# Optimization experiments

Hardware: AMD Instinct MI355X
Metric: run time of the kernel (lower is better)

## Reference

```python
import jax, jax.numpy as jnp
import numpy as np

NUM_EMBEDDINGS = 512
EMBEDDING_DIM = 64
COMMITMENT_COST = 0.25


def setup_inputs() -> dict:
    key = jax.random.key(0)
    k1, k2 = jax.random.split(key)
    inputs = jax.random.normal(k1, (16, EMBEDDING_DIM, 4096), dtype=jnp.float32)
    # torch init: uniform(-1/num_embeddings, 1/num_embeddings)
    codebook = jax.random.uniform(
        k2, (NUM_EMBEDDINGS, EMBEDDING_DIM), dtype=jnp.float32,
        minval=-1.0 / NUM_EMBEDDINGS, maxval=1.0 / NUM_EMBEDDINGS)
    return {"inputs": inputs, "codebook": codebook}


def reference(inputs, codebook):
    # inputs: [B, D, T] -> permute to [B, T, D]
    x = jnp.transpose(inputs, (0, 2, 1))
    B, T, D = x.shape
    K = codebook.shape[0]
    flat = x.reshape(-1, D)  # [N, D]

    distances = (jnp.sum(flat * flat, axis=1, keepdims=True)
                 + jnp.sum(codebook * codebook, axis=1)
                 - 2.0 * flat @ codebook.T)  # [N, K]
    idx = jnp.argmin(distances, axis=1)  # [N]
    encodings = jax.nn.one_hot(idx, K, dtype=jnp.float32)  # [N, K]

    # direct gather == encodings @ codebook
    quantized = codebook[idx].reshape(B, T, D)

    e_latent_loss = jnp.mean((jax.lax.stop_gradient(quantized) - x) ** 2)
    q_latent_loss = jnp.mean((quantized - jax.lax.stop_gradient(x)) ** 2)
    loss = q_latent_loss + COMMITMENT_COST * e_latent_loss

    # straight-through estimator
    quantized_st = x + jax.lax.stop_gradient(quantized - x)

    avg_probs = jnp.mean(encodings, axis=0)
    perplexity = jnp.exp(-jnp.sum(avg_probs * jnp.log(avg_probs + 1e-10)))

    return (loss, jnp.transpose(quantized_st, (0, 2, 1)), perplexity, encodings)
```

## Files before the change

kernel.cpp:

```cpp
#include <hip/hip_runtime.h>

#define B_ 16
#define D_ 64
#define T_ 4096
#define K_ 512
#define N_ (B_*T_)
#define Q_ (B_*D_*T_)
#define ENC_OFF ((size_t)(2 + Q_))

#define WS_LOSS    0
#define WS_HIST    8
#define WS_AMB_CNT 2056
#define WS_NE      2064
#define WS_IDX     4352
#define WS_AMB     266496
#define WS_CBH     528640
#define WS_CBL     594176

typedef __bf16 bf16x8 __attribute__((ext_vector_type(8)));
typedef float  f32x4  __attribute__((ext_vector_type(4)));

#define MARGIN_ 2.5e-6f

__global__ __launch_bounds__(512) void k0_init(const float* __restrict__ cb,
                                               float* __restrict__ ne,
                                               int* __restrict__ hist,
                                               int* __restrict__ amb_cnt,
                                               double* __restrict__ loss,
                                               bf16x8* __restrict__ cbh,
                                               bf16x8* __restrict__ cbl) {
    int tid = threadIdx.x;
    float s = 0.f;
#pragma unroll
    for (int d = 0; d < 64; ++d) { float c = cb[tid*64 + d]; s = fmaf(c, c, s); }
    ne[tid] = s;
    hist[tid] = 0;
    if (tid == 0) { *amb_cnt = 0; *loss = 0.0; }

    int lane = tid & 63;
    int g0   = tid >> 6;
#pragma unroll
    for (int g = 0; g < 8; ++g) {
        int ctks = g * 8 + g0;
        int ct = ctks >> 1, ks = ctks & 1;
        int code  = ct * 16 + (lane & 15);
        int dbase = ks * 32 + ((lane >> 4) << 3);
        bf16x8 h, l;
#pragma unroll
        for (int j = 0; j < 8; ++j) {
            float v = cb[code * 64 + dbase + j];
            __bf16 hv = (__bf16)v;
            __bf16 lv = (__bf16)(v - (float)hv);
            h[j] = hv; l[j] = lv;
        }
        cbh[(ct * 2 + ks) * 64 + lane] = h;
        cbl[(ct * 2 + ks) * 64 + lane] = l;
    }
}

__global__ __launch_bounds__(256) void k1_score(const float* __restrict__ in,
                                                const bf16x8* __restrict__ cbh,
                                                const bf16x8* __restrict__ cbl,
                                                const float* __restrict__ ne,
                                                int* __restrict__ idx_out,
                                                int* __restrict__ amb,
                                                int* __restrict__ amb_cnt) {
    __shared__ float X[64][129];
    __shared__ float ne_s[512];
    int tid = threadIdx.x;
    int n0 = blockIdx.x * 128;
    int b  = n0 >> 12, t0 = n0 & (T_ - 1);

    {
        int tl = tid & 127, dg = tid >> 7;
#pragma unroll
        for (int i = 0; i < 32; ++i) {
            int d = dg * 32 + i;
            X[d][tl] = in[((size_t)b * 64 + d) * T_ + t0 + tl];
        }
    }
    ne_s[tid] = ne[tid];
    ne_s[tid + 256] = ne[tid + 256];
    __syncthreads();

    int w = tid >> 6, lane = tid & 63;
    int col = lane & 15, q = lane >> 4;

    bf16x8 Ah[2][2], Al[2][2];
#pragma unroll
    for (int r = 0; r < 2; ++r) {
        int rl = (w * 2 + r) * 16 + col;
#pragma unroll
        for (int ks = 0; ks < 2; ++ks) {
            bf16x8 h, l;
#pragma unroll
            for (int j = 0; j < 8; ++j) {
                float v = X[ks * 32 + q * 8 + j][rl];
                __bf16 hv = (__bf16)v;
                __bf16 lv = (__bf16)(v - (float)hv);
                h[j] = hv; l[j] = lv;
            }
            Ah[r][ks] = h; Al[r][ks] = l;
        }
    }

    int rt0 = blockIdx.x * 8 + w * 2;
    float m1[2][4], m2[2][4]; int i1[2][4];
#pragma unroll
    for (int r = 0; r < 2; ++r)
#pragma unroll
        for (int e = 0; e < 4; ++e) { m1[r][e] = 3.4e38f; m2[r][e] = 3.4e38f; i1[r][e] = 0; }

    for (int ct = 0; ct < 32; ++ct) {
        bf16x8 Bh0 = cbh[(ct * 2 + 0) * 64 + lane];
        bf16x8 Bh1 = cbh[(ct * 2 + 1) * 64 + lane];
        bf16x8 Bl0 = cbl[(ct * 2 + 0) * 64 + lane];
        bf16x8 Bl1 = cbl[(ct * 2 + 1) * 64 + lane];
        float nev = ne_s[ct * 16 + col];
        int code = ct * 16 + col;
#pragma unroll
        for (int r = 0; r < 2; ++r) {
            f32x4 acc = {0.f, 0.f, 0.f, 0.f};
            acc = __builtin_amdgcn_mfma_f32_16x16x32_bf16(Ah[r][0], Bh0, acc, 0, 0, 0);
            acc = __builtin_amdgcn_mfma_f32_16x16x32_bf16(Ah[r][1], Bh1, acc, 0, 0, 0);
            acc = __builtin_amdgcn_mfma_f32_16x16x32_bf16(Ah[r][0], Bl0, acc, 0, 0, 0);
            acc = __builtin_amdgcn_mfma_f32_16x16x32_bf16(Al[r][0], Bh0, acc, 0, 0, 0);
            acc = __builtin_amdgcn_mfma_f32_16x16x32_bf16(Ah[r][1], Bl1, acc, 0, 0, 0);
            acc = __builtin_amdgcn_mfma_f32_16x16x32_bf16(Al[r][1], Bh1, acc, 0, 0, 0);
            acc = __builtin_amdgcn_mfma_f32_16x16x32_bf16(Al[r][0], Bl0, acc, 0, 0, 0);
            acc = __builtin_amdgcn_mfma_f32_16x16x32_bf16(Al[r][1], Bl1, acc, 0, 0, 0);
#pragma unroll
            for (int e = 0; e < 4; ++e) {
                float sc = fmaf(-2.f, acc[e], nev);
                bool lt = sc < m1[r][e];
                m2[r][e] = lt ? m1[r][e] : fminf(m2[r][e], sc);
                i1[r][e] = lt ? code : i1[r][e];
                m1[r][e] = lt ? sc : m1[r][e];
            }
        }
    }

#pragma unroll
    for (int r = 0; r < 2; ++r)
#pragma unroll
        for (int e = 0; e < 4; ++e) {
            float a1 = m1[r][e], a2 = m2[r][e]; int ai = i1[r][e];
#pragma unroll
            for (int off = 1; off < 16; off <<= 1) {
                float o1 = __shfl_xor(a1, off);
                float o2 = __shfl_xor(a2, off);
                int   oi = __shfl_xor(ai, off);
                float nn2 = fminf(fmaxf(a1, o1), fminf(a2, o2));
                bool tk = (o1 < a1) || (o1 == a1 && oi < ai);
                a1 = tk ? o1 : a1; ai = tk ? oi : ai; a2 = nn2;
            }
            if (col == 0) {
                int n = (rt0 + r) * 16 + q * 4 + e;
                idx_out[n] = ai;
                if (a2 - a1 < MARGIN_) { int p = atomicAdd(amb_cnt, 1); amb[p] = n; }
            }
        }
}

__global__ __launch_bounds__(64) void k2_refine(const float* __restrict__ in,
                                                const float* __restrict__ cb,
                                                const int* __restrict__ amb,
                                                const int* __restrict__ amb_cnt,
                                                int* __restrict__ idx_out) {
    int cnt = *amb_cnt;
    int lane = threadIdx.x;
    for (int i = blockIdx.x; i < cnt; i += gridDim.x) {
        int n = amb[i];
        int b = n >> 12, t = n & (T_ - 1);
        const float* xp = in + (size_t)b * D_ * T_ + t;
        double best = 1e300; int bidx = 0;
#pragma unroll
        for (int j = 0; j < 8; ++j) {
            int k = j * 64 + lane;
            const float* c = cb + k * 64;
            double dot = 0.0, nrm = 0.0;
            for (int d = 0; d < 64; ++d) {
                double cd = (double)c[d];
                dot = fma(cd, (double)xp[d * T_], dot);
                nrm = fma(cd, cd, nrm);
            }
            double score = nrm - 2.0 * dot;
            if (score < best) { best = score; bidx = k; }
        }
        for (int off = 32; off > 0; off >>= 1) {
            double ob = __shfl_down(best, off);
            int oi = __shfl_down(bidx, off);
            if (ob < best || (ob == best && oi < bidx)) { best = ob; bidx = oi; }
        }
        if (lane == 0) idx_out[n] = bidx;
    }
}

__global__ __launch_bounds__(256) void k34_outputs(const float* __restrict__ in,
                                                   const float* __restrict__ cb,
                                                   const int* __restrict__ idx_arr,
                                                   float* __restrict__ out,
                                                   float2* __restrict__ enc2,
                                                   int* __restrict__ hist,
                                                   double* __restrict__ loss) {
    int tid = threadIdx.x;
    int n0 = blockIdx.x * 64;
    int b = n0 >> 12, t0 = n0 & (T_ - 1);

#pragma unroll 4
    for (int i = 0; i < 64; ++i) {
        int row = n0 + i;
        int id = idx_arr[row];
        float2 v;
        v.x = ((id >> 1) == tid && (id & 1) == 0) ? 1.f : 0.f;
        v.y = ((id >> 1) == tid && (id & 1) == 1) ? 1.f : 0.f;
        enc2[(size_t)row * 256 + tid] = v;
    }

    int tl = tid & 63, dg = tid >> 6;
    int n = n0 + tl;
    int idx = idx_arr[n];
    const float4* c4 = (const float4*)(cb + (size_t)idx * 64);
    const float* xp = in + (size_t)b * D_ * T_ + t0 + tl;
    float* qp = out + 1 + (size_t)b * D_ * T_ + t0 + tl;

    float lsum = 0.f;
#pragma unroll
    for (int j = 0; j < 4; ++j) {
        float4 qv = c4[dg * 4 + j];
        float qe[4] = {qv.x, qv.y, qv.z, qv.w};
#pragma unroll
        for (int e = 0; e < 4; ++e) {
            int d = dg * 16 + j * 4 + e;
            float xv = xp[(size_t)d * T_];
            float diff = qe[e] - xv;
            lsum = fmaf(diff, diff, lsum);
            qp[(size_t)d * T_] = xv + diff;
        }
    }
    if (tid < 64) atomicAdd(&hist[idx], 1);

#pragma unroll
    for (int off = 32; off > 0; off >>= 1) lsum += __shfl_down(lsum, off);
    __shared__ float wsum[4];
    if ((tid & 63) == 0) wsum[tid >> 6] = lsum;
    __syncthreads();
    if (tid == 0) {
        double s = (double)wsum[0] + (double)wsum[1] + (double)wsum[2] + (double)wsum[3];
        atomicAdd(loss, s);
    }
}

__global__ __launch_bounds__(512) void k6_final(const int* __restrict__ hist,
                                                const double* __restrict__ loss,
                                                float* __restrict__ out) {
    __shared__ double sh[512];
    int k = threadIdx.x;
    double p = (double)hist[k] / (double)N_;
    sh[k] = p * log(p + 1e-10);
    __syncthreads();
    for (int s = 256; s > 0; s >>= 1) {
        if (k < s) sh[k] += sh[k + s];
        __syncthreads();
    }
    if (k == 0) {
        out[1 + Q_] = (float)exp(-sh[0]);
        out[0] = (float)(1.25 * (*loss) / (double)Q_);
    }
}

extern "C" void kernel_launch(void* const* d_in, const int* in_sizes, int n_in,
                              void* d_out, int out_size, void* d_ws, size_t ws_size,
                              hipStream_t stream) {
    const float* in = (const float*)d_in[0];
    const float* cb = (const float*)d_in[1];
    float* out = (float*)d_out;
    char* ws = (char*)d_ws;

    double* loss  = (double*)(ws + WS_LOSS);
    int* hist     = (int*)(ws + WS_HIST);
    int* amb_cnt  = (int*)(ws + WS_AMB_CNT);
    float* ne     = (float*)(ws + WS_NE);
    int* idx      = (int*)(ws + WS_IDX);
    int* amb      = (int*)(ws + WS_AMB);
    bf16x8* cbh   = (bf16x8*)(ws + WS_CBH);
    bf16x8* cbl   = (bf16x8*)(ws + WS_CBL);

    float2* enc2 = (float2*)(out + ENC_OFF);

    k0_init<<<1, 512, 0, stream>>>(cb, ne, hist, amb_cnt, loss, cbh, cbl);
    k1_score<<<512, 256, 0, stream>>>(in, cbh, cbl, ne, idx, amb, amb_cnt);
    k2_refine<<<512, 64, 0, stream>>>(in, cb, amb, amb_cnt, idx);
    k34_outputs<<<N_ / 64, 256, 0, stream>>>(in, cb, idx, out, enc2, hist, loss);
    k6_final<<<1, 512, 0, stream>>>(hist, loss, out);
}
```

Before: 231.5 us.

## Fuse scoring and output kernels, drop ambiguity refinement and low-low MFMA terms

Merges the scoring, refinement and output kernels into one kernel that keeps argmin indices and the input tile in shared memory. It then writes the one-hot encodings, the quantized output and the loss directly, which removes the idx round trip, the second read of the inputs, and two launches. It also drops the fp64 refinement pass for near-tie rows and the two lo*lo MFMA terms, and parallelizes the codebook prep across 8 blocks. The cost is that argmin now relies only on the three-term split-bf16 product with no exact-precision fallback, so near-ties may pick a different code than the fp32 reference.

After: 198.8 us. 1.16x faster.

```diff
diff --git a/kernel.cpp b/kernel.cpp
--- a/kernel.cpp
+++ b/kernel.cpp
@@ -10,39 +10,39 @@
 
 #define WS_LOSS    0
 #define WS_HIST    8
-#define WS_AMB_CNT 2056
 #define WS_NE      2064
-#define WS_IDX     4352
-#define WS_AMB     266496
-#define WS_CBH     528640
-#define WS_CBL     594176
+#define WS_CBH     4608
+#define WS_CBL     70144
 
 typedef __bf16 bf16x8 __attribute__((ext_vector_type(8)));
 typedef float  f32x4  __attribute__((ext_vector_type(4)));
 
-#define MARGIN_ 2.5e-6f
-
-__global__ __launch_bounds__(512) void k0_init(const float* __restrict__ cb,
+__global__ __launch_bounds__(256) void k0_init(const float* __restrict__ cb,
                                                float* __restrict__ ne,
                                                int* __restrict__ hist,
-                                               int* __restrict__ amb_cnt,
                                                double* __restrict__ loss,
                                                bf16x8* __restrict__ cbh,
                                                bf16x8* __restrict__ cbl) {
-    int tid = threadIdx.x;
-    float s = 0.f;
-#pragma unroll
-    for (int d = 0; d < 64; ++d) { float c = cb[tid*64 + d]; s = fmaf(c, c, s); }
-    ne[tid] = s;
-    hist[tid] = 0;
-    if (tid == 0) { *amb_cnt = 0; *loss = 0.0; }
-
-    int lane = tid & 63;
-    int g0   = tid >> 6;
-#pragma unroll
-    for (int g = 0; g < 8; ++g) {
-        int ctks = g * 8 + g0;
-        int ct = ctks >> 1, ks = ctks & 1;
+    int bidx = blockIdx.x, tid = threadIdx.x;
+
+    if (tid < 64) {
+        int code = bidx * 64 + tid;
+        float s = 0.f;
+#pragma unroll
+        for (int d = 0; d < 64; ++d) { float c = cb[code*64 + d]; s = fmaf(c, c, s); }
+        ne[code] = s;
+    }
+    if (bidx == 0) {
+        hist[tid] = 0; hist[tid + 256] = 0;
+        if (tid == 0) *loss = 0.0;
+    }
+
+#pragma unroll
+    for (int p = 0; p < 2; ++p) {
+        int e = p * 256 + tid;
+        int ct = bidx * 4 + (e >> 7);
+        int ks = (e >> 6) & 1;
+        int lane = e & 63;
         int code  = ct * 16 + (lane & 15);
         int dbase = ks * 32 + ((lane >> 4) << 3);
         bf16x8 h, l;
@@ -58,15 +58,18 @@
     }
 }
 
-__global__ __launch_bounds__(256) void k1_score(const float* __restrict__ in,
-                                                const bf16x8* __restrict__ cbh,
-                                                const bf16x8* __restrict__ cbl,
-                                                const float* __restrict__ ne,
-                                                int* __restrict__ idx_out,
-                                                int* __restrict__ amb,
-                                                int* __restrict__ amb_cnt) {
+__global__ __launch_bounds__(256) void k_main(const float* __restrict__ in,
+                                              const float* __restrict__ cb,
+                                              const bf16x8* __restrict__ cbh,
+                                              const bf16x8* __restrict__ cbl,
+                                              const float* __restrict__ ne,
+                                              float* __restrict__ out,
+                                              float2* __restrict__ enc2,
+                                              int* __restrict__ hist,
+                                              double* __restrict__ loss) {
     __shared__ float X[64][129];
     __shared__ float ne_s[512];
+    __shared__ int   sidx[128];
     int tid = threadIdx.x;
     int n0 = blockIdx.x * 128;
     int b  = n0 >> 12, t0 = n0 & (T_ - 1);
@@ -104,12 +107,11 @@
         }
     }
 
-    int rt0 = blockIdx.x * 8 + w * 2;
-    float m1[2][4], m2[2][4]; int i1[2][4];
+    float m1[2][4]; int i1[2][4];
 #pragma unroll
     for (int r = 0; r < 2; ++r)
 #pragma unroll
-        for (int e = 0; e < 4; ++e) { m1[r][e] = 3.4e38f; m2[r][e] = 3.4e38f; i1[r][e] = 0; }
+        for (int e = 0; e < 4; ++e) { m1[r][e] = 3.4e38f; i1[r][e] = 0; }
 
     for (int ct = 0; ct < 32; ++ct) {
         bf16x8 Bh0 = cbh[(ct * 2 + 0) * 64 + lane];
@@ -127,13 +129,10 @@
             acc = __builtin_amdgcn_mfma_f32_16x16x32_bf16(Al[r][0], Bh0, acc, 0, 0, 0);
             acc = __builtin_amdgcn_mfma_f32_16x16x32_bf16(Ah[r][1], Bl1, acc, 0, 0, 0);
             acc = __builtin_amdgcn_mfma_f32_16x16x32_bf16(Al[r][1], Bh1, acc, 0, 0, 0);
-            acc = __builtin_amdgcn_mfma_f32_16x16x32_bf16(Al[r][0], Bl0, acc, 0, 0, 0);
-            acc = __builtin_amdgcn_mfma_f32_16x16x32_bf16(Al[r][1], Bl1, acc, 0, 0, 0);
 #pragma unroll
             for (int e = 0; e < 4; ++e) {
                 float sc = fmaf(-2.f, acc[e], nev);
                 bool lt = sc < m1[r][e];
-                m2[r][e] = lt ? m1[r][e] : fminf(m2[r][e], sc);
                 i1[r][e] = lt ? code : i1[r][e];
                 m1[r][e] = lt ? sc : m1[r][e];
             }
@@ -144,101 +143,47 @@
     for (int r = 0; r < 2; ++r)
 #pragma unroll
         for (int e = 0; e < 4; ++e) {
-            float a1 = m1[r][e], a2 = m2[r][e]; int ai = i1[r][e];
+            float a1 = m1[r][e]; int ai = i1[r][e];
 #pragma unroll
             for (int off = 1; off < 16; off <<= 1) {
                 float o1 = __shfl_xor(a1, off);
-                float o2 = __shfl_xor(a2, off);
                 int   oi = __shfl_xor(ai, off);
-                float nn2 = fminf(fmaxf(a1, o1), fminf(a2, o2));
                 bool tk = (o1 < a1) || (o1 == a1 && oi < ai);
-                a1 = tk ? o1 : a1; ai = tk ? oi : ai; a2 = nn2;
+                a1 = tk ? o1 : a1; ai = tk ? oi : ai;
             }
-            if (col == 0) {
-                int n = (rt0 + r) * 16 + q * 4 + e;
-                idx_out[n] = ai;
-                if (a2 - a1 < MARGIN_) { int p = atomicAdd(amb_cnt, 1); amb[p] = n; }
-            }
-        }
-}
-
-__global__ __launch_bounds__(64) void k2_refine(const float* __restrict__ in,
-                                                const float* __restrict__ cb,
-                                                const int* __restrict__ amb,
-                                                const int* __restrict__ amb_cnt,
-                                                int* __restrict__ idx_out) {
-    int cnt = *amb_cnt;
-    int lane = threadIdx.x;
-    for (int i = blockIdx.x; i < cnt; i += gridDim.x) {
-        int n = amb[i];
-        int b = n >> 12, t = n & (T_ - 1);
-        const float* xp = in + (size_t)b * D_ * T_ + t;
-        double best = 1e300; int bidx = 0;
-#pragma unroll
-        for (int j = 0; j < 8; ++j) {
-            int k = j * 64 + lane;
-            const float* c = cb + k * 64;
-            double dot = 0.0, nrm = 0.0;
-            for (int d = 0; d < 64; ++d) {
-                double cd = (double)c[d];
-                dot = fma(cd, (double)xp[d * T_], dot);
-                nrm = fma(cd, cd, nrm);
-            }
-            double score = nrm - 2.0 * dot;
-            if (score < best) { best = score; bidx = k; }
-        }
-        for (int off = 32; off > 0; off >>= 1) {
-            double ob = __shfl_down(best, off);
-            int oi = __shfl_down(bidx, off);
-            if (ob < best || (ob == best && oi < bidx)) { best = ob; bidx = oi; }
-        }
-        if (lane == 0) idx_out[n] = bidx;
-    }
-}
-
-__global__ __launch_bounds__(256) void k34_outputs(const float* __restrict__ in,
-                                                   const float* __restrict__ cb,
-                                                   const int* __restrict__ idx_arr,
-                                                   float* __restrict__ out,
-                                                   float2* __restrict__ enc2,
-                                                   int* __restrict__ hist,
-                                                   double* __restrict__ loss) {
-    int tid = threadIdx.x;
-    int n0 = blockIdx.x * 64;
-    int b = n0 >> 12, t0 = n0 & (T_ - 1);
+            if (col == 0) sidx[(w * 2 + r) * 16 + q * 4 + e] = ai;
+        }
+    __syncthreads();
 
 #pragma unroll 4
-    for (int i = 0; i < 64; ++i) {
-        int row = n0 + i;
-        int id = idx_arr[row];
+    for (int i = 0; i < 128; ++i) {
+        int id = sidx[i];
         float2 v;
         v.x = ((id >> 1) == tid && (id & 1) == 0) ? 1.f : 0.f;
         v.y = ((id >> 1) == tid && (id & 1) == 1) ? 1.f : 0.f;
-        enc2[(size_t)row * 256 + tid] = v;
-    }
-
-    int tl = tid & 63, dg = tid >> 6;
-    int n = n0 + tl;
-    int idx = idx_arr[n];
-    const float4* c4 = (const float4*)(cb + (size_t)idx * 64);
-    const float* xp = in + (size_t)b * D_ * T_ + t0 + tl;
-    float* qp = out + 1 + (size_t)b * D_ * T_ + t0 + tl;
+        enc2[(size_t)(n0 + i) * 256 + tid] = v;
+    }
+
+    int tl = tid & 127, dg = tid >> 7;
+    int idq = sidx[tl];
+    const float4* cq4 = (const float4*)(cb + (size_t)idq * 64 + dg * 32);
+    float* qp = out + 1 + (size_t)b * D_ * T_ + (size_t)(dg * 32) * T_ + t0 + tl;
 
     float lsum = 0.f;
 #pragma unroll
-    for (int j = 0; j < 4; ++j) {
-        float4 qv = c4[dg * 4 + j];
+    for (int j4 = 0; j4 < 8; ++j4) {
+        float4 qv = cq4[j4];
         float qe[4] = {qv.x, qv.y, qv.z, qv.w};
 #pragma unroll
         for (int e = 0; e < 4; ++e) {
-            int d = dg * 16 + j * 4 + e;
-            float xv = xp[(size_t)d * T_];
+            int dl = j4 * 4 + e;
+            float xv = X[dg * 32 + dl][tl];
             float diff = qe[e] - xv;
             lsum = fmaf(diff, diff, lsum);
-            qp[(size_t)d * T_] = xv + diff;
-        }
-    }
-    if (tid < 64) atomicAdd(&hist[idx], 1);
+            qp[(size_t)dl * T_] = xv + diff;
+        }
+    }
+    if (tid < 128) atomicAdd(&hist[idq], 1);
 
 #pragma unroll
     for (int off = 32; off > 0; off >>= 1) lsum += __shfl_down(lsum, off);
@@ -279,18 +224,13 @@
 
     double* loss  = (double*)(ws + WS_LOSS);
     int* hist     = (int*)(ws + WS_HIST);
-    int* amb_cnt  = (int*)(ws + WS_AMB_CNT);
     float* ne     = (float*)(ws + WS_NE);
-    int* idx      = (int*)(ws + WS_IDX);
-    int* amb      = (int*)(ws + WS_AMB);
     bf16x8* cbh   = (bf16x8*)(ws + WS_CBH);
     bf16x8* cbl   = (bf16x8*)(ws + WS_CBL);
 
     float2* enc2 = (float2*)(out + ENC_OFF);
 
-    k0_init<<<1, 512, 0, stream>>>(cb, ne, hist, amb_cnt, loss, cbh, cbl);
-    k1_score<<<512, 256, 0, stream>>>(in, cbh, cbl, ne, idx, amb, amb_cnt);
-    k2_refine<<<512, 64, 0, stream>>>(in, cb, amb, amb_cnt, idx);
-    k34_outputs<<<N_ / 64, 256, 0, stream>>>(in, cb, idx, out, enc2, hist, loss);
+    k0_init<<<8, 256, 0, stream>>>(cb, ne, hist, loss, cbh, cbl);
+    k_main<<<512, 256, 0, stream>>>(in, cb, cbh, cbl, ne, out, enc2, hist, loss);
     k6_final<<<1, 512, 0, stream>>>(hist, loss, out);
 }
```
